# Optimization experiments

Hardware: AMD Instinct MI355X
Metric: run time of the kernel (lower is better)

Reference implementation:

```python
import jax, jax.numpy as jnp
import numpy as np

D = 768      # embed_dim
L = 12       # depth
H = 12       # num_heads
NF = 8       # max num_frames
P = 16       # patch size
IMG = 224
N = (IMG // P) ** 2   # 196 patches per frame
HID = 4 * D
EPS = 1e-6


def layernorm(x, s, b):
    m = x.mean(-1, keepdims=True)
    v = ((x - m) ** 2).mean(-1, keepdims=True)
    return (x - m) * jax.lax.rsqrt(v + EPS) * s + b


def _attn(q, k, v):
    sim = jnp.einsum('bid,bjd->bij', q, k)
    a = jax.nn.softmax(sim, axis=-1)
    return jnp.einsum('bij,bjd->bid', a, v)


def var_attention(x, qkv_w, qkv_b, proj_w, proj_b, f, n, mode):
    """Divided space/time attention with CLS broadcast (VarAttention)."""
    B, S, Dm = x.shape
    h = H
    d = Dm // h
    scale = d ** -0.5
    qkv = x @ qkv_w.T + qkv_b
    q, k, v = jnp.split(qkv, 3, axis=-1)

    def heads(t):  # b n (h d) -> (b h) n d
        return t.reshape(B, S, h, d).transpose(0, 2, 1, 3).reshape(B * h, S, d)

    q, k, v = heads(q) * scale, heads(k), heads(v)
    cls_q, q_ = q[:, :1], q[:, 1:]
    cls_k, k_ = k[:, :1], k[:, 1:]
    cls_v, v_ = v[:, :1], v[:, 1:]
    cls_out = _attn(cls_q, k, v)  # CLS attends to everything
    Bh = B * h
    if mode == 'space':   # b (f n) d -> (b f) n d
        q_, k_, v_ = [t.reshape(Bh * f, n, d) for t in (q_, k_, v_)]
        r = f
    else:                 # time: b (f n) d -> (b n) f d
        q_, k_, v_ = [t.reshape(Bh, f, n, d).transpose(0, 2, 1, 3).reshape(Bh * n, f, d)
                      for t in (q_, k_, v_)]
        r = n
    ck = jnp.repeat(cls_k, r, axis=0)  # b () d -> (b r) () d
    cv = jnp.repeat(cls_v, r, axis=0)
    out = _attn(q_, jnp.concatenate([ck, k_], axis=1), jnp.concatenate([cv, v_], axis=1))
    if mode == 'space':
        out = out.reshape(Bh, f * n, d)
    else:
        out = out.reshape(Bh, n, f, d).transpose(0, 2, 1, 3).reshape(Bh, f * n, d)
    out = jnp.concatenate([cls_out, out], axis=1)
    out = out.reshape(B, h, S, d).transpose(0, 2, 1, 3).reshape(B, S, Dm)
    return out @ proj_w.T + proj_b


def setup_inputs() -> dict:
    key = jax.random.key(0)
    ks = iter(jax.random.split(key, 40))
    s = 0.02
    B, F = 4, 8
    inp = {
        'x': jax.random.normal(next(ks), (B, F, 3, IMG, IMG), jnp.float32),
        'patch_w': jax.random.normal(next(ks), (D, 3, P, P), jnp.float32) * s,
        'patch_b': jnp.zeros((D,), jnp.float32),
        'cls_token': jax.random.normal(next(ks), (1, 1, D), jnp.float32) * s,
        'pos_embed': jax.random.normal(next(ks), (1, N + 1, D), jnp.float32) * s,
        'temporal_embed': jax.random.normal(next(ks), (1, NF, D), jnp.float32) * s,
        'norm1_s': jnp.ones((L, D), jnp.float32), 'norm1_b': jnp.zeros((L, D), jnp.float32),
        'norm2_s': jnp.ones((L, D), jnp.float32), 'norm2_b': jnp.zeros((L, D), jnp.float32),
        'norm3_s': jnp.ones((L, D), jnp.float32), 'norm3_b': jnp.zeros((L, D), jnp.float32),
        'attn_qkv_w': jax.random.normal(next(ks), (L, 3 * D, D), jnp.float32) * s,
        'attn_qkv_b': jnp.zeros((L, 3 * D), jnp.float32),
        'attn_proj_w': jax.random.normal(next(ks), (L, D, D), jnp.float32) * s,
        'attn_proj_b': jnp.zeros((L, D), jnp.float32),
        'time_qkv_w': jax.random.normal(next(ks), (L, 3 * D, D), jnp.float32) * s,
        'time_qkv_b': jnp.zeros((L, 3 * D), jnp.float32),
        'time_proj_w': jax.random.normal(next(ks), (L, D, D), jnp.float32) * s,
        'time_proj_b': jnp.zeros((L, D), jnp.float32),
        'fc1_w': jax.random.normal(next(ks), (L, HID, D), jnp.float32) * s,
        'fc1_b': jnp.zeros((L, HID), jnp.float32),
        'fc2_w': jax.random.normal(next(ks), (L, D, HID), jnp.float32) * s,
        'fc2_b': jnp.zeros((L, D), jnp.float32),
        'norm_s': jnp.ones((D,), jnp.float32), 'norm_b': jnp.zeros((D,), jnp.float32),
    }
    return inp


def reference(x, patch_w, patch_b, cls_token, pos_embed, temporal_embed,
              norm1_s, norm1_b, norm2_s, norm2_b, norm3_s, norm3_b,
              attn_qkv_w, attn_qkv_b, attn_proj_w, attn_proj_b,
              time_qkv_w, time_qkv_b, time_proj_w, time_proj_b,
              fc1_w, fc1_b, fc2_w, fc2_b, norm_s, norm_b):
    B, F, C, Hh, Ww = x.shape
    nh, nw = Hh // P, Ww // P
    # patch embed: stride=kernel conv as patch-flatten + matmul
    xp = x.reshape(B * F, C, nh, P, nw, P).transpose(0, 2, 4, 1, 3, 5)
    xp = xp.reshape(B * F, nh * nw, C * P * P)
    xp = xp @ patch_w.reshape(D, C * P * P).T + patch_b   # [BF, N, D]
    xt = xp.reshape(B, F * nh * nw, D)
    cls = jnp.broadcast_to(cls_token, (B, 1, D))
    xt = jnp.concatenate([cls, xt], axis=1)               # [B, 1+F*N, D]
    # positional embedding: spatial tiled over frames, temporal repeated within frame
    cls_embed = pos_embed[:, :1]
    tile_pos = jnp.tile(pos_embed[:, 1:], (1, NF, 1))
    tile_temp = jnp.repeat(temporal_embed, N, axis=1)
    total = jnp.concatenate([cls_embed, tile_pos + tile_temp], axis=1)
    xt = xt + total[:, :xt.shape[1]]
    n, f = N, F
    for i in range(L):
        t_out = var_attention(layernorm(xt, norm3_s[i], norm3_b[i]),
                              time_qkv_w[i], time_qkv_b[i], time_proj_w[i], time_proj_b[i],
                              f, n, 'time')
        time_res = xt + t_out
        s_out = var_attention(layernorm(time_res, norm1_s[i], norm1_b[i]),
                              attn_qkv_w[i], attn_qkv_b[i], attn_proj_w[i], attn_proj_b[i],
                              f, n, 'space')
        space_res = xt + s_out  # frozen-in-time: residual from original x
        hdn = jax.nn.gelu(layernorm(space_res, norm2_s[i], norm2_b[i]) @ fc1_w[i].T + fc1_b[i],
                          approximate=False)
        xt = space_res + hdn @ fc2_w[i].T + fc2_b[i]
    xt = layernorm(xt, norm_s, norm_b)
    return xt[:, 0]   # [B, D] CLS features
```

## Files before the change

kernel.cpp:

```cpp
#include <hip/hip_runtime.h>
#include <hip/hip_bf16.h>


#define DEV __device__ __forceinline__

typedef __bf16 bf16x8 __attribute__((ext_vector_type(8)));
typedef float f32x4 __attribute__((ext_vector_type(4)));

static constexpr int D = 768;
static constexpr int S = 1569;
static constexpr int B = 4;
static constexpr int NH = 12;
static constexpr int NF = 8;
static constexpr int NP = 196;
static constexpr int M  = B * S;
static constexpr int Mp = 6400;

DEV void gload16(const void* g, void* l) {
  __builtin_amdgcn_global_load_lds((const __attribute__((address_space(1))) void*)g,
                                   (__attribute__((address_space(3))) void*)l, 16, 0, 0);
}

DEV ushort f2bfu(float f) {
  __hip_bfloat16 h = __float2bfloat16(f);
  return *reinterpret_cast<ushort*>(&h);
}

template<int EPI>
__global__ __launch_bounds__(256)
void gemm_bt(const __hip_bfloat16* __restrict__ A,
             const __hip_bfloat16* __restrict__ Bw,
             const float* __restrict__ bias,
             const float* __restrict__ res,
             float* __restrict__ Cf,
             __hip_bfloat16* __restrict__ Cb,
             int N, int K)
{
  __shared__ __hip_bfloat16 As[128 * 64];
  __shared__ __hip_bfloat16 Bs[128 * 64];
  const int tid  = threadIdx.x;
  const int lane = tid & 63;
  const int wave = tid >> 6;
  const int wm = wave >> 1, wn = wave & 1;
  const int bm = blockIdx.y * 128, bn = blockIdx.x * 128;

  const int srow = lane >> 3;
  const int scol = (lane & 7) * 8;

  const int lrow = lane & 15;
  const int lk   = (lane >> 4) * 8;

  f32x4 acc[4][4] = {};

  for (int k0 = 0; k0 < K; k0 += 64) {
    #pragma unroll
    for (int c = 0; c < 4; ++c) {
      const int r = wave * 32 + c * 8;
      gload16(A  + (size_t)(bm + r + srow) * K + k0 + scol, &As[r * 64]);
      gload16(Bw + (size_t)(bn + r + srow) * K + k0 + scol, &Bs[r * 64]);
    }
    __syncthreads();
    #pragma unroll
    for (int kk = 0; kk < 2; ++kk) {
      bf16x8 af[4], bfr[4];
      #pragma unroll
      for (int m = 0; m < 4; ++m)
        af[m] = *reinterpret_cast<const bf16x8*>(&As[(wm*64 + m*16 + lrow)*64 + kk*32 + lk]);
      #pragma unroll
      for (int n = 0; n < 4; ++n)
        bfr[n] = *reinterpret_cast<const bf16x8*>(&Bs[(wn*64 + n*16 + lrow)*64 + kk*32 + lk]);
      #pragma unroll
      for (int m = 0; m < 4; ++m)
        #pragma unroll
        for (int n = 0; n < 4; ++n)
          acc[m][n] = __builtin_amdgcn_mfma_f32_16x16x32_bf16(af[m], bfr[n], acc[m][n], 0, 0, 0);
    }
    __syncthreads();
  }

  const int crow0 = bm + wm*64 + (lane >> 4) * 4;
  const int ccol0 = bn + wn*64 + (lane & 15);
  #pragma unroll
  for (int m = 0; m < 4; ++m) {
    #pragma unroll
    for (int n = 0; n < 4; ++n) {
      #pragma unroll
      for (int i = 0; i < 4; ++i) {
        const int row = crow0 + m*16 + i;
        const int col = ccol0 + n*16;
        const size_t off = (size_t)row * N + col;
        float v = acc[m][n][i] + bias[col];
        if (EPI == 1) {
          Cf[off] = v + res[off];
        } else if (EPI == 2) {
          float g = 0.5f * v * (1.0f + erff(v * 0.70710678118654752f));
          Cb[off] = __float2bfloat16(g);
        } else {
          Cf[off] = v;
        }
      }
    }
  }
}

__global__ __launch_bounds__(256)
void ln_bf16_kernel(const float* __restrict__ in, const float* __restrict__ sc,
                    const float* __restrict__ bb, __hip_bfloat16* __restrict__ out)
{
  __shared__ float red[4];
  const int row = blockIdx.x, tid = threadIdx.x;
  const float* x = in + (size_t)row * D;
  float x0 = x[tid], x1 = x[tid + 256], x2 = x[tid + 512];
  float s = x0 + x1 + x2;
  for (int o = 32; o; o >>= 1) s += __shfl_down(s, o);
  if ((tid & 63) == 0) red[tid >> 6] = s;
  __syncthreads();
  const float mean = (red[0] + red[1] + red[2] + red[3]) * (1.f / 768.f);
  __syncthreads();
  const float d0 = x0 - mean, d1 = x1 - mean, d2 = x2 - mean;
  float v = d0*d0 + d1*d1 + d2*d2;
  for (int o = 32; o; o >>= 1) v += __shfl_down(v, o);
  if ((tid & 63) == 0) red[tid >> 6] = v;
  __syncthreads();
  const float var = (red[0] + red[1] + red[2] + red[3]) * (1.f / 768.f);
  const float r = rsqrtf(var + 1e-6f);
  __hip_bfloat16* orow = out + (size_t)row * D;
  orow[tid]       = __float2bfloat16(d0 * r * sc[tid]       + bb[tid]);
  orow[tid + 256] = __float2bfloat16(d1 * r * sc[tid + 256] + bb[tid + 256]);
  orow[tid + 512] = __float2bfloat16(d2 * r * sc[tid + 512] + bb[tid + 512]);
}

__global__ __launch_bounds__(256)
void ln_final_kernel(const float* __restrict__ in, const float* __restrict__ sc,
                     const float* __restrict__ bb, float* __restrict__ out)
{
  __shared__ float red[4];
  const int b = blockIdx.x, tid = threadIdx.x;
  const float* x = in + (size_t)(b * S) * D;
  float x0 = x[tid], x1 = x[tid + 256], x2 = x[tid + 512];
  float s = x0 + x1 + x2;
  for (int o = 32; o; o >>= 1) s += __shfl_down(s, o);
  if ((tid & 63) == 0) red[tid >> 6] = s;
  __syncthreads();
  const float mean = (red[0] + red[1] + red[2] + red[3]) * (1.f / 768.f);
  __syncthreads();
  const float d0 = x0 - mean, d1 = x1 - mean, d2 = x2 - mean;
  float v = d0*d0 + d1*d1 + d2*d2;
  for (int o = 32; o; o >>= 1) v += __shfl_down(v, o);
  if ((tid & 63) == 0) red[tid >> 6] = v;
  __syncthreads();
  const float var = (red[0] + red[1] + red[2] + red[3]) * (1.f / 768.f);
  const float r = rsqrtf(var + 1e-6f);
  float* orow = out + (size_t)b * D;
  orow[tid]       = d0 * r * sc[tid]       + bb[tid];
  orow[tid + 256] = d1 * r * sc[tid + 256] + bb[tid + 256];
  orow[tid + 512] = d2 * r * sc[tid + 512] + bb[tid + 512];
}

__global__ __launch_bounds__(256)
void cls_attn_kernel(const float* __restrict__ qkv, __hip_bfloat16* __restrict__ out)
{
  __shared__ float qs[64];
  __shared__ float sims[S];
  __shared__ float opart[4][64];
  __shared__ float red[4];
  const int b = blockIdx.x / NH, h = blockIdx.x % NH;
  const int tid = threadIdx.x;
  const float* base = qkv + (size_t)b * S * 2304;
  if (tid < 64) qs[tid] = base[h * 64 + tid] * 0.125f;
  __syncthreads();
  float lmax = -1e30f;
  for (int j = tid; j < S; j += 256) {
    const float* kr = base + (size_t)j * 2304 + 768 + h * 64;
    float sacc = 0.f;
    #pragma unroll
    for (int c = 0; c < 16; ++c) {
      float4 kv = *(const float4*)(kr + c * 4);
      sacc += qs[c*4+0]*kv.x + qs[c*4+1]*kv.y + qs[c*4+2]*kv.z + qs[c*4+3]*kv.w;
    }
    sims[j] = sacc;
    lmax = fmaxf(lmax, sacc);
  }
  for (int o = 32; o; o >>= 1) lmax = fmaxf(lmax, __shfl_down(lmax, o));
  if ((tid & 63) == 0) red[tid >> 6] = lmax;
  __syncthreads();
  const float m = fmaxf(fmaxf(red[0], red[1]), fmaxf(red[2], red[3]));
  __syncthreads();
  float lsum = 0.f;
  for (int j = tid; j < S; j += 256) {
    float p = __expf(sims[j] - m);
    sims[j] = p;
    lsum += p;
  }
  for (int o = 32; o; o >>= 1) lsum += __shfl_down(lsum, o);
  if ((tid & 63) == 0) red[tid >> 6] = lsum;
  __syncthreads();
  const float l = red[0] + red[1] + red[2] + red[3];
  const int wave = tid >> 6, lane = tid & 63;
  float oa = 0.f;
  for (int j = wave; j < S; j += 4) {
    const float* vr = base + (size_t)j * 2304 + 1536 + h * 64;
    oa += sims[j] * vr[lane];
  }
  opart[wave][lane] = oa;
  __syncthreads();
  if (tid < 64) {
    float o = (opart[0][tid] + opart[1][tid] + opart[2][tid] + opart[3][tid]) / l;
    out[(size_t)(b * S) * D + h * 64 + tid] = __float2bfloat16(o);
  }
}

__global__ __launch_bounds__(256)
void time_attn_kernel(const float* __restrict__ qkv, __hip_bfloat16* __restrict__ out)
{
  __shared__ float Ks[4][9][64];
  __shared__ float Vs[4][9][64];
  const int tid = threadIdx.x;
  const int grp = tid >> 6, lane = tid & 63;
  const int g = blockIdx.x * 4 + grp;
  const int n = g % NP;
  const int h = (g / NP) % NH;
  const int b = g / (NP * NH);
  const float* base = qkv + (size_t)b * S * 2304;
  #pragma unroll
  for (int j = 0; j < 9; ++j) {
    const int sj = (j == 0) ? 0 : (1 + (j - 1) * NP + n);
    const float* r = base + (size_t)sj * 2304 + h * 64;
    Ks[grp][j][lane] = r[768 + lane];
    Vs[grp][j][lane] = r[1536 + lane];
  }
  const int qi = lane >> 3, sub = lane & 7;
  const int sq = 1 + qi * NP + n;
  const float* qp = base + (size_t)sq * 2304 + h * 64 + sub * 8;
  float4 q0 = *(const float4*)qp;
  float4 q1 = *(const float4*)(qp + 4);
  float qf[8] = {q0.x, q0.y, q0.z, q0.w, q1.x, q1.y, q1.z, q1.w};
  #pragma unroll
  for (int t = 0; t < 8; ++t) qf[t] *= 0.125f;
  __syncthreads();
  float sim[9];
  #pragma unroll
  for (int j = 0; j < 9; ++j) {
    float p = 0.f;
    #pragma unroll
    for (int t = 0; t < 8; ++t) p += qf[t] * Ks[grp][j][sub * 8 + t];
    p += __shfl_xor(p, 1, 8);
    p += __shfl_xor(p, 2, 8);
    p += __shfl_xor(p, 4, 8);
    sim[j] = p;
  }
  float m = sim[0];
  #pragma unroll
  for (int j = 1; j < 9; ++j) m = fmaxf(m, sim[j]);
  float l = 0.f;
  #pragma unroll
  for (int j = 0; j < 9; ++j) { sim[j] = __expf(sim[j] - m); l += sim[j]; }
  const float inv = 1.f / l;
  float o[8] = {};
  #pragma unroll
  for (int j = 0; j < 9; ++j)
    #pragma unroll
    for (int t = 0; t < 8; ++t) o[t] += sim[j] * Vs[grp][j][sub * 8 + t];
  union { ushort us[8]; uint4 v; } pk;
  #pragma unroll
  for (int t = 0; t < 8; ++t) pk.us[t] = f2bfu(o[t] * inv);
  *(uint4*)(out + (size_t)(b * S + sq) * D + h * 64 + sub * 8) = pk.v;
}

__global__ __launch_bounds__(256, 2)
void space_attn_kernel(const float* __restrict__ qkv, __hip_bfloat16* __restrict__ out)
{
  __shared__ __hip_bfloat16 Ks[197][64];
  __shared__ __hip_bfloat16 Vs[197][64];
  const int tid = threadIdx.x;
  const int f = blockIdx.x & 7;
  const int h = (blockIdx.x >> 3) % NH;
  const int b = blockIdx.x / (NH * NF);
  const float* base = qkv + (size_t)b * S * 2304;
  for (int idx = tid; idx < 197 * 8; idx += 256) {
    const int j = idx >> 3, c = (idx & 7) * 8;
    const int sj = (j == 0) ? 0 : (1 + f * NP + j - 1);
    const float* r = base + (size_t)sj * 2304 + h * 64 + c;
    float4 k0 = *(const float4*)(r + 768);
    float4 k1 = *(const float4*)(r + 772);
    float4 v0 = *(const float4*)(r + 1536);
    float4 v1 = *(const float4*)(r + 1540);
    __hip_bfloat16* kp = &Ks[j][c];
    kp[0] = __float2bfloat16(k0.x); kp[1] = __float2bfloat16(k0.y);
    kp[2] = __float2bfloat16(k0.z); kp[3] = __float2bfloat16(k0.w);
    kp[4] = __float2bfloat16(k1.x); kp[5] = __float2bfloat16(k1.y);
    kp[6] = __float2bfloat16(k1.z); kp[7] = __float2bfloat16(k1.w);
    __hip_bfloat16* vp = &Vs[j][c];
    vp[0] = __float2bfloat16(v0.x); vp[1] = __float2bfloat16(v0.y);
    vp[2] = __float2bfloat16(v0.z); vp[3] = __float2bfloat16(v0.w);
    vp[4] = __float2bfloat16(v1.x); vp[5] = __float2bfloat16(v1.y);
    vp[6] = __float2bfloat16(v1.z); vp[7] = __float2bfloat16(v1.w);
  }
  __syncthreads();
  const int n = tid;
  if (n < NP) {
    const int sq = 1 + f * NP + n;
    const float* qp = base + (size_t)sq * 2304 + h * 64;
    float qf[64];
    #pragma unroll
    for (int c = 0; c < 16; ++c) {
      float4 q = *(const float4*)(qp + c * 4);
      qf[c*4+0] = q.x * 0.125f; qf[c*4+1] = q.y * 0.125f;
      qf[c*4+2] = q.z * 0.125f; qf[c*4+3] = q.w * 0.125f;
    }
    float m = -1e30f, l = 0.f;
    float o[64] = {};
    for (int j = 0; j < 197; ++j) {
      const uint* kr = (const uint*)&Ks[j][0];
      float sacc = 0.f;
      #pragma unroll
      for (int c = 0; c < 32; ++c) {
        const uint u = kr[c];
        sacc += qf[2*c]   * __uint_as_float(u << 16);
        sacc += qf[2*c+1] * __uint_as_float(u & 0xffff0000u);
      }
      if (sacc > m + 8.f) {
        const float corr = __expf(m - sacc);
        l *= corr;
        #pragma unroll
        for (int dd = 0; dd < 64; ++dd) o[dd] *= corr;
        m = sacc;
      }
      const float p = __expf(sacc - m);
      l += p;
      const uint* vr = (const uint*)&Vs[j][0];
      #pragma unroll
      for (int c = 0; c < 32; ++c) {
        const uint u = vr[c];
        o[2*c]   += p * __uint_as_float(u << 16);
        o[2*c+1] += p * __uint_as_float(u & 0xffff0000u);
      }
    }
    const float inv = 1.f / l;
    __hip_bfloat16* orow = out + (size_t)(b * S + sq) * D + h * 64;
    #pragma unroll
    for (int c8 = 0; c8 < 8; ++c8) {
      union { ushort us[8]; uint4 v; } pk;
      #pragma unroll
      for (int t = 0; t < 8; ++t) pk.us[t] = f2bfu(o[c8 * 8 + t] * inv);
      *(uint4*)(orow + c8 * 8) = pk.v;
    }
  }
}

__global__ __launch_bounds__(256)
void im2col_kernel(const float* __restrict__ x, __hip_bfloat16* __restrict__ A)
{
  const int idx = blockIdx.x * 256 + threadIdx.x;
  const int col = idx % 768;
  const int row = idx / 768;
  const int px = col & 15, py = (col >> 4) & 15, c = col >> 8;
  const int pw = row % 14, ph = (row / 14) % 14, bf = row / 196;
  const float v = x[(((size_t)bf * 3 + c) * 224 + ph * 16 + py) * 224 + pw * 16 + px];
  A[idx] = __float2bfloat16(v);
}

__global__ __launch_bounds__(256)
void assemble_kernel(const float* __restrict__ xp, const float* __restrict__ cls,
                     const float* __restrict__ pos, const float* __restrict__ temb,
                     float* __restrict__ xt)
{
  const int idx = blockIdx.x * 256 + threadIdx.x;
  const int d = idx % D;
  const int s = (idx / D) % S;
  const int b = idx / (D * S);
  float v;
  if (s == 0) {
    v = cls[d] + pos[d];
  } else {
    const int j = s - 1, f = j / NP, nn = j % NP;
    v = xp[((size_t)(b * NF + f) * NP + nn) * D + d]
        + pos[(size_t)(1 + nn) * D + d] + temb[(size_t)f * D + d];
  }
  xt[((size_t)b * S + s) * D + d] = v;
}

__global__ __launch_bounds__(256)
void wconv6_kernel(const float* __restrict__ tq, const float* __restrict__ tp,
                   const float* __restrict__ aq, const float* __restrict__ ap,
                   const float* __restrict__ f1, const float* __restrict__ f2,
                   __hip_bfloat16* __restrict__ dst)
{
  const size_t i = ((size_t)blockIdx.x * 256 + threadIdx.x) * 4;
  const float* src;
  size_t off = i;
  if      (i < 1769472u) { src = tq; }
  else if (i < 2359296u) { src = tp; off = i - 1769472u; }
  else if (i < 4128768u) { src = aq; off = i - 2359296u; }
  else if (i < 4718592u) { src = ap; off = i - 4128768u; }
  else if (i < 7077888u) { src = f1; off = i - 4718592u; }
  else                   { src = f2; off = i - 7077888u; }
  const float4 v = *(const float4*)(src + off);
  union { ushort us[4]; uint2 u; } pk;
  pk.us[0] = f2bfu(v.x); pk.us[1] = f2bfu(v.y);
  pk.us[2] = f2bfu(v.z); pk.us[3] = f2bfu(v.w);
  *(uint2*)(dst + i) = pk.u;
}

__global__ __launch_bounds__(256)
void wconv1_kernel(const float* __restrict__ src, __hip_bfloat16* __restrict__ dst)
{
  const size_t i = ((size_t)blockIdx.x * 256 + threadIdx.x) * 4;
  const float4 v = *(const float4*)(src + i);
  union { ushort us[4]; uint2 u; } pk;
  pk.us[0] = f2bfu(v.x); pk.us[1] = f2bfu(v.y);
  pk.us[2] = f2bfu(v.z); pk.us[3] = f2bfu(v.w);
  *(uint2*)(dst + i) = pk.u;
}

extern "C" void kernel_launch(void* const* d_in, const int* in_sizes, int n_in,
                              void* d_out, int out_size, void* d_ws, size_t ws_size,
                              hipStream_t stream) {
  (void)in_sizes; (void)n_in; (void)out_size; (void)ws_size;
  const float* x       = (const float*)d_in[0];
  const float* patch_w = (const float*)d_in[1];
  const float* patch_b = (const float*)d_in[2];
  const float* cls_t   = (const float*)d_in[3];
  const float* pos_e   = (const float*)d_in[4];
  const float* tem_e   = (const float*)d_in[5];
  const float* n1s = (const float*)d_in[6];
  const float* n1b = (const float*)d_in[7];
  const float* n2s = (const float*)d_in[8];
  const float* n2b = (const float*)d_in[9];
  const float* n3s = (const float*)d_in[10];
  const float* n3b = (const float*)d_in[11];
  const float* aqw = (const float*)d_in[12];
  const float* aqb = (const float*)d_in[13];
  const float* apw = (const float*)d_in[14];
  const float* apb = (const float*)d_in[15];
  const float* tqw = (const float*)d_in[16];
  const float* tqb = (const float*)d_in[17];
  const float* tpw = (const float*)d_in[18];
  const float* tpb = (const float*)d_in[19];
  const float* f1w = (const float*)d_in[20];
  const float* f1b = (const float*)d_in[21];
  const float* f2w = (const float*)d_in[22];
  const float* f2b = (const float*)d_in[23];
  const float* nfs = (const float*)d_in[24];
  const float* nfb = (const float*)d_in[25];
  float* outp = (float*)d_out;

  char* ws = (char*)d_ws;
  float* xt  = (float*)(ws);
  float* rs  = (float*)(ws + 19660800);
  float* qkv = (float*)(ws + 39321600);
  __hip_bfloat16* abf = (__hip_bfloat16*)(ws + 98304000);
  __hip_bfloat16* wbf = (__hip_bfloat16*)(ws + 137625600);
  __hip_bfloat16* hdn = (__hip_bfloat16*)qkv;

  const size_t O_TQ = 0, O_TP = 1769472, O_AQ = 2359296, O_AP = 4128768,
               O_F1 = 4718592, O_F2 = 7077888;

  im2col_kernel<<<18816, 256, 0, stream>>>(x, abf);
  wconv1_kernel<<<576, 256, 0, stream>>>(patch_w, wbf);
  gemm_bt<0><<<dim3(6, 49), 256, 0, stream>>>(abf, wbf, patch_b, nullptr, qkv, nullptr, 768, 768);
  assemble_kernel<<<18828, 256, 0, stream>>>(qkv, cls_t, pos_e, tem_e, xt);

  for (int i = 0; i < 12; ++i) {
    wconv6_kernel<<<9216, 256, 0, stream>>>(
        tqw + (size_t)i * 1769472, tpw + (size_t)i * 589824,
        aqw + (size_t)i * 1769472, apw + (size_t)i * 589824,
        f1w + (size_t)i * 2359296, f2w + (size_t)i * 2359296, wbf);

    ln_bf16_kernel<<<M, 256, 0, stream>>>(xt, n3s + i * 768, n3b + i * 768, abf);
    gemm_bt<0><<<dim3(18, 50), 256, 0, stream>>>(abf, wbf + O_TQ, tqb + (size_t)i * 2304,
                                                 nullptr, qkv, nullptr, 2304, 768);
    cls_attn_kernel<<<48, 256, 0, stream>>>(qkv, abf);
    time_attn_kernel<<<2352, 256, 0, stream>>>(qkv, abf);
    gemm_bt<1><<<dim3(6, 50), 256, 0, stream>>>(abf, wbf + O_TP, tpb + (size_t)i * 768,
                                                xt, rs, nullptr, 768, 768);

    ln_bf16_kernel<<<M, 256, 0, stream>>>(rs, n1s + i * 768, n1b + i * 768, abf);
    gemm_bt<0><<<dim3(18, 50), 256, 0, stream>>>(abf, wbf + O_AQ, aqb + (size_t)i * 2304,
                                                 nullptr, qkv, nullptr, 2304, 768);
    cls_attn_kernel<<<48, 256, 0, stream>>>(qkv, abf);
    space_attn_kernel<<<384, 256, 0, stream>>>(qkv, abf);
    gemm_bt<1><<<dim3(6, 50), 256, 0, stream>>>(abf, wbf + O_AP, apb + (size_t)i * 768,
                                                xt, rs, nullptr, 768, 768);

    ln_bf16_kernel<<<M, 256, 0, stream>>>(rs, n2s + i * 768, n2b + i * 768, abf);
    gemm_bt<2><<<dim3(24, 50), 256, 0, stream>>>(abf, wbf + O_F1, f1b + (size_t)i * 3072,
                                                 nullptr, nullptr, hdn, 3072, 768);
    gemm_bt<1><<<dim3(6, 50), 256, 0, stream>>>(hdn, wbf + O_F2, f2b + (size_t)i * 768,
                                                rs, xt, nullptr, 768, 3072);
  }

  ln_final_kernel<<<4, 256, 0, stream>>>(xt, nfs, nfb, outp);
}
```

Measured before the change: 9.279 ms.

## Use MFMA f16 for space attention and one-wave-per-row layernorm

Replaces the scalar per-thread online-softmax space attention with a tiled MFMA implementation. K is stored swizzled and V transposed in LDS as f16, and a full-row softmax writes probabilities to LDS for a second MFMA against V. Layernorm is rewritten so each wavefront handles one row with vectorized loads and shuffle reductions, removing block syncs and LDS. Switching attention inputs to f16 changes numerical precision versus the prior bf16/f32 path.

```diff
diff --git a/kernel.cpp b/kernel.cpp
--- a/kernel.cpp
+++ b/kernel.cpp
@@ -6,6 +6,9 @@
 
 typedef __bf16 bf16x8 __attribute__((ext_vector_type(8)));
 typedef float f32x4 __attribute__((ext_vector_type(4)));
+typedef _Float16 f16;
+typedef _Float16 f16x8 __attribute__((ext_vector_type(8)));
+typedef _Float16 f16x4 __attribute__((ext_vector_type(4)));
 
 static constexpr int D = 768;
 static constexpr int S = 1569;
@@ -14,7 +17,6 @@
 static constexpr int NF = 8;
 static constexpr int NP = 196;
 static constexpr int M  = B * S;
-static constexpr int Mp = 6400;
 
 DEV void gload16(const void* g, void* l) {
   __builtin_amdgcn_global_load_lds((const __attribute__((address_space(1))) void*)g,
@@ -107,27 +109,40 @@
 void ln_bf16_kernel(const float* __restrict__ in, const float* __restrict__ sc,
                     const float* __restrict__ bb, __hip_bfloat16* __restrict__ out)
 {
-  __shared__ float red[4];
-  const int row = blockIdx.x, tid = threadIdx.x;
+  const int tid = threadIdx.x, w = tid >> 6, lane = tid & 63;
+  const int row = blockIdx.x * 4 + w;
   const float* x = in + (size_t)row * D;
-  float x0 = x[tid], x1 = x[tid + 256], x2 = x[tid + 512];
-  float s = x0 + x1 + x2;
-  for (int o = 32; o; o >>= 1) s += __shfl_down(s, o);
-  if ((tid & 63) == 0) red[tid >> 6] = s;
-  __syncthreads();
-  const float mean = (red[0] + red[1] + red[2] + red[3]) * (1.f / 768.f);
-  __syncthreads();
-  const float d0 = x0 - mean, d1 = x1 - mean, d2 = x2 - mean;
-  float v = d0*d0 + d1*d1 + d2*d2;
-  for (int o = 32; o; o >>= 1) v += __shfl_down(v, o);
-  if ((tid & 63) == 0) red[tid >> 6] = v;
-  __syncthreads();
-  const float var = (red[0] + red[1] + red[2] + red[3]) * (1.f / 768.f);
-  const float r = rsqrtf(var + 1e-6f);
+  const int c0 = lane * 4;
+  float4 v0 = *(const float4*)(x + c0);
+  float4 v1 = *(const float4*)(x + 256 + c0);
+  float4 v2 = *(const float4*)(x + 512 + c0);
+  float s = v0.x+v0.y+v0.z+v0.w + v1.x+v1.y+v1.z+v1.w + v2.x+v2.y+v2.z+v2.w;
+  #pragma unroll
+  for (int o = 32; o; o >>= 1) s += __shfl_xor(s, o);
+  const float mean = s * (1.f / 768.f);
+  float var = 0.f;
+  #define SQ(t) { float d_ = (t) - mean; var += d_*d_; }
+  SQ(v0.x) SQ(v0.y) SQ(v0.z) SQ(v0.w)
+  SQ(v1.x) SQ(v1.y) SQ(v1.z) SQ(v1.w)
+  SQ(v2.x) SQ(v2.y) SQ(v2.z) SQ(v2.w)
+  #undef SQ
+  #pragma unroll
+  for (int o = 32; o; o >>= 1) var += __shfl_xor(var, o);
+  const float r = rsqrtf(var * (1.f / 768.f) + 1e-6f);
   __hip_bfloat16* orow = out + (size_t)row * D;
-  orow[tid]       = __float2bfloat16(d0 * r * sc[tid]       + bb[tid]);
-  orow[tid + 256] = __float2bfloat16(d1 * r * sc[tid + 256] + bb[tid + 256]);
-  orow[tid + 512] = __float2bfloat16(d2 * r * sc[tid + 512] + bb[tid + 512]);
+  #pragma unroll
+  for (int c = 0; c < 3; ++c) {
+    const int col = c * 256 + c0;
+    float4 vv = (c == 0) ? v0 : (c == 1) ? v1 : v2;
+    float4 sv = *(const float4*)(sc + col);
+    float4 bv = *(const float4*)(bb + col);
+    union { ushort us[4]; uint2 u; } pk;
+    pk.us[0] = f2bfu((vv.x - mean) * r * sv.x + bv.x);
+    pk.us[1] = f2bfu((vv.y - mean) * r * sv.y + bv.y);
+    pk.us[2] = f2bfu((vv.z - mean) * r * sv.z + bv.z);
+    pk.us[3] = f2bfu((vv.w - mean) * r * sv.w + bv.w);
+    *(uint2*)(orow + col) = pk.u;
+  }
 }
 
 __global__ __launch_bounds__(256)
@@ -267,83 +282,118 @@
   *(uint4*)(out + (size_t)(b * S + sq) * D + h * 64 + sub * 8) = pk.v;
 }
 
+DEV f16* kls_addr(f16* basep, int key, int colb) {
+  return (f16*)((char*)basep + key * 128 + (colb ^ ((key & 7) << 4)));
+}
+
 __global__ __launch_bounds__(256, 2)
 void space_attn_kernel(const float* __restrict__ qkv, __hip_bfloat16* __restrict__ out)
 {
-  __shared__ __hip_bfloat16 Ks[197][64];
-  __shared__ __hip_bfloat16 Vs[197][64];
+  __shared__ f16 Kls[208 * 64];
+  __shared__ f16 Vt[64 * 208];
+  __shared__ f16 Pls[4][16 * 208];
+
   const int tid = threadIdx.x;
   const int f = blockIdx.x & 7;
   const int h = (blockIdx.x >> 3) % NH;
   const int b = blockIdx.x / (NH * NF);
   const float* base = qkv + (size_t)b * S * 2304;
-  for (int idx = tid; idx < 197 * 8; idx += 256) {
-    const int j = idx >> 3, c = (idx & 7) * 8;
-    const int sj = (j == 0) ? 0 : (1 + f * NP + j - 1);
-    const float* r = base + (size_t)sj * 2304 + h * 64 + c;
-    float4 k0 = *(const float4*)(r + 768);
-    float4 k1 = *(const float4*)(r + 772);
-    float4 v0 = *(const float4*)(r + 1536);
-    float4 v1 = *(const float4*)(r + 1540);
-    __hip_bfloat16* kp = &Ks[j][c];
-    kp[0] = __float2bfloat16(k0.x); kp[1] = __float2bfloat16(k0.y);
-    kp[2] = __float2bfloat16(k0.z); kp[3] = __float2bfloat16(k0.w);
-    kp[4] = __float2bfloat16(k1.x); kp[5] = __float2bfloat16(k1.y);
-    kp[6] = __float2bfloat16(k1.z); kp[7] = __float2bfloat16(k1.w);
-    __hip_bfloat16* vp = &Vs[j][c];
-    vp[0] = __float2bfloat16(v0.x); vp[1] = __float2bfloat16(v0.y);
-    vp[2] = __float2bfloat16(v0.z); vp[3] = __float2bfloat16(v0.w);
-    vp[4] = __float2bfloat16(v1.x); vp[5] = __float2bfloat16(v1.y);
-    vp[6] = __float2bfloat16(v1.z); vp[7] = __float2bfloat16(v1.w);
-  }
-  __syncthreads();
-  const int n = tid;
-  if (n < NP) {
-    const int sq = 1 + f * NP + n;
-    const float* qp = base + (size_t)sq * 2304 + h * 64;
-    float qf[64];
-    #pragma unroll
-    for (int c = 0; c < 16; ++c) {
-      float4 q = *(const float4*)(qp + c * 4);
-      qf[c*4+0] = q.x * 0.125f; qf[c*4+1] = q.y * 0.125f;
-      qf[c*4+2] = q.z * 0.125f; qf[c*4+3] = q.w * 0.125f;
-    }
-    float m = -1e30f, l = 0.f;
-    float o[64] = {};
-    for (int j = 0; j < 197; ++j) {
-      const uint* kr = (const uint*)&Ks[j][0];
-      float sacc = 0.f;
-      #pragma unroll
-      for (int c = 0; c < 32; ++c) {
-        const uint u = kr[c];
-        sacc += qf[2*c]   * __uint_as_float(u << 16);
-        sacc += qf[2*c+1] * __uint_as_float(u & 0xffff0000u);
+
+  for (int idx = tid; idx < 208 * 8; idx += 256) {
+    const int key = idx >> 3, ch = idx & 7;
+    float k8[8] = {}, v8[8] = {};
+    if (key < 197) {
+      const int row = (key == 0) ? 0 : 1 + f * NP + key - 1;
+      const float* kr = base + (size_t)row * 2304 + 768 + h * 64 + ch * 8;
+      float4 a = *(const float4*)kr, b2 = *(const float4*)(kr + 4);
+      k8[0]=a.x; k8[1]=a.y; k8[2]=a.z; k8[3]=a.w;
+      k8[4]=b2.x; k8[5]=b2.y; k8[6]=b2.z; k8[7]=b2.w;
+      float4 c1 = *(const float4*)(kr + 768), c2 = *(const float4*)(kr + 772);
+      v8[0]=c1.x; v8[1]=c1.y; v8[2]=c1.z; v8[3]=c1.w;
+      v8[4]=c2.x; v8[5]=c2.y; v8[6]=c2.z; v8[7]=c2.w;
+    }
+    f16x8 kp;
+    #pragma unroll
+    for (int j = 0; j < 8; ++j) kp[j] = (f16)k8[j];
+    *(f16x8*)kls_addr(Kls, key, ch * 16) = kp;
+    #pragma unroll
+    for (int j = 0; j < 8; ++j) Vt[(ch * 8 + j) * 208 + key] = (f16)v8[j];
+  }
+  __syncthreads();
+
+  const int w = tid >> 6, lane = tid & 63;
+  const int l15 = lane & 15, g = lane >> 4;
+  f16* Pw = &Pls[w][0];
+
+  for (int Qt = w; Qt < 13; Qt += 4) {
+    const int qidx = Qt * 16 + l15;
+    const float* qp = base + (size_t)(1 + f * NP + qidx) * 2304 + h * 64 + g * 8;
+    f16x8 q0, q1;
+    {
+      float4 a = *(const float4*)qp, b2 = *(const float4*)(qp + 4);
+      float4 c1 = *(const float4*)(qp + 32), c2 = *(const float4*)(qp + 36);
+      q0[0]=(f16)(a.x*0.125f); q0[1]=(f16)(a.y*0.125f); q0[2]=(f16)(a.z*0.125f); q0[3]=(f16)(a.w*0.125f);
+      q0[4]=(f16)(b2.x*0.125f); q0[5]=(f16)(b2.y*0.125f); q0[6]=(f16)(b2.z*0.125f); q0[7]=(f16)(b2.w*0.125f);
+      q1[0]=(f16)(c1.x*0.125f); q1[1]=(f16)(c1.y*0.125f); q1[2]=(f16)(c1.z*0.125f); q1[3]=(f16)(c1.w*0.125f);
+      q1[4]=(f16)(c2.x*0.125f); q1[5]=(f16)(c2.y*0.125f); q1[6]=(f16)(c2.z*0.125f); q1[7]=(f16)(c2.w*0.125f);
+    }
+    f32x4 sacc[13] = {};
+    #pragma unroll
+    for (int kt = 0; kt < 13; ++kt) {
+      const int key = kt * 16 + l15;
+      f16x8 a0 = *(const f16x8*)kls_addr(Kls, key, g * 16);
+      f16x8 a1 = *(const f16x8*)kls_addr(Kls, key, 64 + g * 16);
+      sacc[kt] = __builtin_amdgcn_mfma_f32_16x16x32_f16(a0, q0, sacc[kt], 0, 0, 0);
+      sacc[kt] = __builtin_amdgcn_mfma_f32_16x16x32_f16(a1, q1, sacc[kt], 0, 0, 0);
+    }
+    #pragma unroll
+    for (int i = 0; i < 4; ++i)
+      if (g * 4 + i >= 5) sacc[12][i] = -1e30f;
+    float mx = -1e30f;
+    #pragma unroll
+    for (int kt = 0; kt < 13; ++kt)
+      #pragma unroll
+      for (int i = 0; i < 4; ++i) mx = fmaxf(mx, sacc[kt][i]);
+    mx = fmaxf(mx, __shfl_xor(mx, 16));
+    mx = fmaxf(mx, __shfl_xor(mx, 32));
+    float sum = 0.f;
+    #pragma unroll
+    for (int kt = 0; kt < 13; ++kt) {
+      f16x4 pk;
+      #pragma unroll
+      for (int i = 0; i < 4; ++i) {
+        float p = __expf(sacc[kt][i] - mx);
+        sum += p;
+        pk[i] = (f16)p;
       }
-      if (sacc > m + 8.f) {
-        const float corr = __expf(m - sacc);
-        l *= corr;
+      *(f16x4*)&Pw[l15 * 208 + kt * 16 + g * 4] = pk;
+    }
+    sum += __shfl_xor(sum, 16);
+    sum += __shfl_xor(sum, 32);
+    const float linv = 1.f / sum;
+    f32x4 oacc[4] = {};
+    #pragma unroll
+    for (int kt2 = 0; kt2 < 7; ++kt2) {
+      const bool tail = (kt2 == 6) && (g >= 2);
+      f16x8 pa = {};
+      if (!tail) pa = *(const f16x8*)&Pw[l15 * 208 + kt2 * 32 + g * 8];
+      #pragma unroll
+      for (int dt = 0; dt < 4; ++dt) {
+        f16x8 vb = {};
+        if (!tail) vb = *(const f16x8*)&Vt[(dt * 16 + l15) * 208 + kt2 * 32 + g * 8];
+        oacc[dt] = __builtin_amdgcn_mfma_f32_16x16x32_f16(pa, vb, oacc[dt], 0, 0, 0);
+      }
+    }
+    #pragma unroll
+    for (int i = 0; i < 4; ++i) {
+      const float lv = __shfl(linv, g * 4 + i);
+      const int qo = Qt * 16 + g * 4 + i;
+      if (qo < NP) {
+        __hip_bfloat16* orow = out + (size_t)(b * S + 1 + f * NP + qo) * D + h * 64 + l15;
         #pragma unroll
-        for (int dd = 0; dd < 64; ++dd) o[dd] *= corr;
-        m = sacc;
+        for (int dt = 0; dt < 4; ++dt)
+          orow[dt * 16] = __float2bfloat16(oacc[dt][i] * lv);
       }
-      const float p = __expf(sacc - m);
-      l += p;
-      const uint* vr = (const uint*)&Vs[j][0];
-      #pragma unroll
-      for (int c = 0; c < 32; ++c) {
-        const uint u = vr[c];
-        o[2*c]   += p * __uint_as_float(u << 16);
-        o[2*c+1] += p * __uint_as_float(u & 0xffff0000u);
-      }
-    }
-    const float inv = 1.f / l;
-    __hip_bfloat16* orow = out + (size_t)(b * S + sq) * D + h * 64;
-    #pragma unroll
-    for (int c8 = 0; c8 < 8; ++c8) {
-      union { ushort us[8]; uint4 v; } pk;
-      #pragma unroll
-      for (int t = 0; t < 8; ++t) pk.us[t] = f2bfu(o[c8 * 8 + t] * inv);
-      *(uint4*)(orow + c8 * 8) = pk.v;
     }
   }
 }
@@ -467,7 +517,7 @@
         aqw + (size_t)i * 1769472, apw + (size_t)i * 589824,
         f1w + (size_t)i * 2359296, f2w + (size_t)i * 2359296, wbf);
 
-    ln_bf16_kernel<<<M, 256, 0, stream>>>(xt, n3s + i * 768, n3b + i * 768, abf);
+    ln_bf16_kernel<<<1569, 256, 0, stream>>>(xt, n3s + i * 768, n3b + i * 768, abf);
     gemm_bt<0><<<dim3(18, 50), 256, 0, stream>>>(abf, wbf + O_TQ, tqb + (size_t)i * 2304,
                                                  nullptr, qkv, nullptr, 2304, 768);
     cls_attn_kernel<<<48, 256, 0, stream>>>(qkv, abf);
@@ -475,7 +525,7 @@
     gemm_bt<1><<<dim3(6, 50), 256, 0, stream>>>(abf, wbf + O_TP, tpb + (size_t)i * 768,
                                                 xt, rs, nullptr, 768, 768);
 
-    ln_bf16_kernel<<<M, 256, 0, stream>>>(rs, n1s + i * 768, n1b + i * 768, abf);
+    ln_bf16_kernel<<<1569, 256, 0, stream>>>(rs, n1s + i * 768, n1b + i * 768, abf);
     gemm_bt<0><<<dim3(18, 50), 256, 0, stream>>>(abf, wbf + O_AQ, aqb + (size_t)i * 2304,
                                                  nullptr, qkv, nullptr, 2304, 768);
     cls_attn_kernel<<<48, 256, 0, stream>>>(qkv, abf);
@@ -483,7 +533,7 @@
     gemm_bt<1><<<dim3(6, 50), 256, 0, stream>>>(abf, wbf + O_AP, apb + (size_t)i * 768,
                                                 xt, rs, nullptr, 768, 768);
 
-    ln_bf16_kernel<<<M, 256, 0, stream>>>(rs, n2s + i * 768, n2b + i * 768, abf);
+    ln_bf16_kernel<<<1569, 256, 0, stream>>>(rs, n2s + i * 768, n2b + i * 768, abf);
     gemm_bt<2><<<dim3(24, 50), 256, 0, stream>>>(abf, wbf + O_F1, f1b + (size_t)i * 3072,
                                                  nullptr, nullptr, hdn, 3072, 768);
     gemm_bt<1><<<dim3(6, 50), 256, 0, stream>>>(hdn, wbf + O_F2, f2b + (size_t)i * 768,
```

Measured after the change: 7.435 ms. 19.9% less time.
